# Kernel optimization log

Measured on AMD Instinct MI355X. Metric: run time of the kernel, lower is better.

## Reference

```python
import jax, jax.numpy as jnp
import numpy as np


def setup_inputs() -> dict:
    key = jax.random.key(0)
    k1, k2, k3, k4 = jax.random.split(key, 4)
    B, T, E, H, D = 4, 2048, 1024, 16, 64
    x = jax.random.normal(k1, (B, T, E), dtype=jnp.float32)
    # wv stored as [E, H*D] so y = x @ wv (math-equivalent to nn.Linear weight.T)
    wv = jax.random.normal(k2, (E, H * D), dtype=jnp.float32) * (1.0 / E) ** 0.5
    wr = jax.random.normal(k3, (H, E, T), dtype=jnp.float32) * (2.0 / E) ** 0.5
    wo = jax.random.normal(k4, (H * D, E), dtype=jnp.float32) * (1.0 / (H * D)) ** 0.5
    return {"x": x, "wv": wv, "wr": wr, "wo": wo}


def reference(x, wv, wr, wo):
    B, T, E = x.shape
    H = wr.shape[0]
    HD = wv.shape[1]
    D = HD // H
    # values: [B, H, T, D]
    v = (x @ wv).reshape(B, T, H, D).transpose(0, 2, 1, 3)
    # per-key scores, identical for every query row: s[b,h,k]
    s = jnp.einsum('bte,het->bht', x, wr[:, :, :T]) / jnp.sqrt(jnp.asarray(D, x.dtype))
    # causal softmax over keys k<=q with scores shared across queries reduces to
    # a prefix-softmax-weighted cumulative sum over V (exact same math, O(T)):
    # out[q] = sum_{k<=q} exp(s_k - m) v_k / sum_{k<=q} exp(s_k - m)
    m = jnp.max(s, axis=-1, keepdims=True)          # global max is a valid stable shift
    e = jnp.exp(s - m)                              # [B,H,T]
    num = jnp.cumsum(e[..., None] * v, axis=2)      # [B,H,T,D]
    den = jnp.cumsum(e, axis=2)[..., None]          # [B,H,T,1]
    out = num / den                                 # [B,H,T,D]
    out = out.transpose(0, 2, 1, 3).reshape(B, T, HD)
    return out @ wo
```

## Files before the change

### kernel.cpp

```cpp
#include <hip/hip_runtime.h>
#include <stdint.h>

typedef unsigned short u16;
typedef __attribute__((ext_vector_type(8))) short short8;
typedef __attribute__((ext_vector_type(8))) unsigned short ushort8v;
typedef __attribute__((ext_vector_type(4))) float f32x4;

#define B_  4
#define T_  2048
#define E_  1024
#define H_  16
#define D_  64
#define HD_ 1024
#define BT_ (B_*T_)
#define TC_ 64
#define NC_ (T_/TC_)
#define SG_ 32
#define SEB_ (E_/SG_)
#define SHB_ 2

__device__ __forceinline__ u16 f2b(float f) {
  uint32_t u = __float_as_uint(f);
  uint32_t r = (u + 0x7FFFu + ((u >> 16) & 1u)) >> 16;
  return (u16)r;
}
__device__ __forceinline__ float b2f(u16 u) {
  return __uint_as_float(((uint32_t)u) << 16);
}

__global__ __launch_bounds__(256) void prep_all(const float* __restrict__ x,
                                                const float* __restrict__ wv,
                                                const float* __restrict__ wo,
                                                u16* __restrict__ xb,
                                                u16* __restrict__ xTb8,
                                                u16* __restrict__ wvT,
                                                u16* __restrict__ woT) {
  __shared__ float tile[64][65];
  const int bid = blockIdx.x;
  if (bid < 2048) {
    const int b = bid >> 9, rest = bid & 511;
    const int t0 = (rest >> 4) * 64, e0 = (rest & 15) * 64;
    const int c4 = (threadIdx.x & 15) * 4;
    const int rw = threadIdx.x >> 4;
#pragma unroll
    for (int r = 0; r < 4; ++r) {
      const int row = r * 16 + rw;
      const float4 v4 = *reinterpret_cast<const float4*>(
          &x[((size_t)b * T_ + t0 + row) * E_ + e0 + c4]);
      tile[row][c4 + 0] = v4.x; tile[row][c4 + 1] = v4.y;
      tile[row][c4 + 2] = v4.z; tile[row][c4 + 3] = v4.w;
      ushort4 o;
      o.x = f2b(v4.x); o.y = f2b(v4.y); o.z = f2b(v4.z); o.w = f2b(v4.w);
      *reinterpret_cast<ushort4*>(&xb[((size_t)(b * T_ + t0 + row)) * E_ + e0 + c4]) = o;
    }
    __syncthreads();
    const int tl = threadIdx.x & 63;
    const int eg = threadIdx.x >> 6;
#pragma unroll
    for (int p = 0; p < 2; ++p) {
      const int egg = eg + p * 4;
      ushort8v o;
#pragma unroll
      for (int j = 0; j < 8; ++j) o[j] = f2b(tile[tl][egg * 8 + j]);
      *reinterpret_cast<ushort8v*>(
          &xTb8[((size_t)(b * (E_ / 8) + (e0 >> 3) + egg) * T_ + t0 + tl) * 8]) = o;
    }
  } else {
    const int k = bid - 2048;
    const float* in = (k >> 8) ? wo : wv;
    u16* out = (k >> 8) ? woT : wvT;
    const int r0 = ((k >> 4) & 15) * 64, c0 = (k & 15) * 64;
    const int tx = threadIdx.x & 63, ty = threadIdx.x >> 6;
#pragma unroll
    for (int r = 0; r < 16; ++r) {
      int row = r * 4 + ty;
      tile[row][tx] = in[(size_t)(r0 + row) * 1024 + c0 + tx];
    }
    __syncthreads();
#pragma unroll
    for (int r = 0; r < 16; ++r) {
      int row = r * 4 + ty;
      out[(size_t)(c0 + row) * 1024 + r0 + tx] = f2b(tile[tx][row]);
    }
  }
}

template <int OUT_BF16>
__global__ __launch_bounds__(256) void gemm_bt(const u16* __restrict__ A,
                                               const u16* __restrict__ Bt,
                                               float* __restrict__ Cf,
                                               u16* __restrict__ Cb,
                                               int M, int N, int K) {
  __shared__ __align__(16) u16 As[2][128 * 64];
  __shared__ __align__(16) u16 Bs[2][128 * 64];
  const int tid  = threadIdx.x;
  const int lane = tid & 63;
  const int wave = tid >> 6;
  const int wr_  = wave >> 1, wc_ = wave & 1;

  const int nwg = gridDim.x * gridDim.y;
  const int bid = blockIdx.y * gridDim.x + blockIdx.x;
  const int cpx = nwg >> 3;
  const int swz = (bid & 7) * cpx + (bid >> 3);
  const int bx = swz % gridDim.x, by = swz / gridDim.x;
  const int brow = by * 128;
  const int bcol = bx * 128;
  const int l15 = lane & 15, l4 = lane >> 4;

  f32x4 acc[4][4];
  const f32x4 zero = {0.f, 0.f, 0.f, 0.f};
#pragma unroll
  for (int i = 0; i < 4; ++i)
#pragma unroll
    for (int j = 0; j < 4; ++j) acc[i][j] = zero;

  auto stage = [&](int kt, int buf) {
    const int k0 = kt * 64;
#pragma unroll
    for (int s2 = 0; s2 < 4; ++s2) {
      const int c = s2 * 256 + tid;
      const int row = c >> 3, g = c & 7;
      const int gs = g ^ (row & 7);
      const u16* ga = A  + (size_t)(brow + row) * K + k0 + gs * 8;
      const u16* gb = Bt + (size_t)(bcol + row) * K + k0 + gs * 8;
      u16* la = &As[buf][(size_t)(s2 * 256 + wave * 64) * 8];
      u16* lb = &Bs[buf][(size_t)(s2 * 256 + wave * 64) * 8];
      __builtin_amdgcn_global_load_lds((const __attribute__((address_space(1))) void*)ga,
                                       (__attribute__((address_space(3))) void*)la,
                                       16, 0, 0);
      __builtin_amdgcn_global_load_lds((const __attribute__((address_space(1))) void*)gb,
                                       (__attribute__((address_space(3))) void*)lb,
                                       16, 0, 0);
    }
  };

  const int NK = K / 64;
  stage(0, 0);
  __syncthreads();

  int cur = 0;
  for (int kt = 0; kt < NK; ++kt) {
    if (kt + 1 < NK) stage(kt + 1, cur ^ 1);

    short8 af[2][4], bfr[2][4];
#pragma unroll
    for (int kk = 0; kk < 2; ++kk) {
      const int sg = (kk * 4 + l4) ^ (l15 & 7);
#pragma unroll
      for (int mi = 0; mi < 4; ++mi)
        af[kk][mi] = *reinterpret_cast<const short8*>(
            &As[cur][(wr_ * 64 + mi * 16 + l15) * 64 + sg * 8]);
#pragma unroll
      for (int ni = 0; ni < 4; ++ni)
        bfr[kk][ni] = *reinterpret_cast<const short8*>(
            &Bs[cur][(wc_ * 64 + ni * 16 + l15) * 64 + sg * 8]);
    }
    __builtin_amdgcn_s_setprio(1);
#pragma unroll
    for (int kk = 0; kk < 2; ++kk)
#pragma unroll
      for (int mi = 0; mi < 4; ++mi)
#pragma unroll
        for (int ni = 0; ni < 4; ++ni)
          acc[mi][ni] = __builtin_amdgcn_mfma_f32_16x16x32_bf16(af[kk][mi], bfr[kk][ni],
                                                                acc[mi][ni], 0, 0, 0);
    __builtin_amdgcn_s_setprio(0);
    __syncthreads();
    cur ^= 1;
  }

#pragma unroll
  for (int mi = 0; mi < 4; ++mi) {
#pragma unroll
    for (int ni = 0; ni < 4; ++ni) {
      const int col = bcol + wc_ * 64 + ni * 16 + l15;
#pragma unroll
      for (int j = 0; j < 4; ++j) {
        const int row = brow + wr_ * 64 + mi * 16 + l4 * 4 + j;
        if (OUT_BF16) Cb[(size_t)row * N + col] = f2b(acc[mi][ni][j]);
        else          Cf[(size_t)row * N + col] = acc[mi][ni][j];
      }
    }
  }
}

__global__ __launch_bounds__(256) void score_partial(const u16* __restrict__ xTb8,
                                                     const float* __restrict__ wr,
                                                     u16* __restrict__ partial) {
  const int t  = blockIdx.x * 256 + threadIdx.x;
  const int g  = blockIdx.y;
  const int h0 = blockIdx.z * SHB_;
  float acc[4][SHB_];
#pragma unroll
  for (int b = 0; b < 4; ++b)
#pragma unroll
    for (int hh = 0; hh < SHB_; ++hh) acc[b][hh] = 0.f;

#pragma unroll
  for (int e8 = 0; e8 < SEB_ / 8; ++e8) {
    const int eb = g * (SEB_ / 8) + e8;
    ushort8v xv[4];
#pragma unroll
    for (int b = 0; b < 4; ++b)
      xv[b] = *reinterpret_cast<const ushort8v*>(
          &xTb8[((size_t)(b * (E_ / 8) + eb) * T_ + t) * 8]);
#pragma unroll
    for (int j = 0; j < 8; ++j) {
      const int e = eb * 8 + j;
      float xf[4];
#pragma unroll
      for (int b = 0; b < 4; ++b) xf[b] = b2f(xv[b][j]);
#pragma unroll
      for (int hh = 0; hh < SHB_; ++hh) {
        const float w = wr[((size_t)(h0 + hh) * E_ + e) * T_ + t];
#pragma unroll
        for (int b = 0; b < 4; ++b) acc[b][hh] = fmaf(xf[b], w, acc[b][hh]);
      }
    }
  }
  u16* pp = partial + (size_t)g * (B_ * H_ * T_);
#pragma unroll
  for (int b = 0; b < 4; ++b)
#pragma unroll
    for (int hh = 0; hh < SHB_; ++hh)
      pp[((size_t)b * H_ + h0 + hh) * T_ + t] = f2b(acc[b][hh] * 0.125f);
}

__global__ __launch_bounds__(256) void chunk_sums(const u16* __restrict__ partial,
                                                  const u16* __restrict__ v,
                                                  float* __restrict__ s,
                                                  float* __restrict__ sev,
                                                  float* __restrict__ se,
                                                  float* __restrict__ mc) {
  const int bh = blockIdx.y;
  const int b = bh >> 4, h = bh & 15;
  const int w = threadIdx.x >> 6, d = threadIdx.x & 63;
  const int c = blockIdx.x * 4 + w;
  const int t = blockIdx.x * 256 + threadIdx.x;

  float sv = 0.f;
#pragma unroll
  for (int g = 0; g < SG_; ++g)
    sv += b2f(partial[(size_t)g * (B_ * H_ * T_) + (size_t)bh * T_ + t]);
  s[(size_t)bh * T_ + t] = sv;

  __shared__ float es[4][64];
  es[w][d] = sv;

  float lm = sv;
#pragma unroll
  for (int off = 1; off < 64; off <<= 1) lm = fmaxf(lm, __shfl_xor(lm, off, 64));

  const u16* vp = v + ((size_t)(b * T_ + c * TC_)) * HD_ + h * D_ + d;
  float acc = 0.f, ae = 0.f;
#pragma unroll 8
  for (int tt = 0; tt < TC_; ++tt) {
    float e = __expf(es[w][tt] - lm);
    acc = fmaf(e, b2f(vp[(size_t)tt * HD_]), acc);
    ae += e;
  }
  sev[((size_t)bh * NC_ + c) * D_ + d] = acc;
  if (d == 0) { se[bh * NC_ + c] = ae; mc[bh * NC_ + c] = lm; }
}

__global__ __launch_bounds__(256) void chunk_scan(const float* __restrict__ s,
                                                  const u16* __restrict__ v,
                                                  const float* __restrict__ sev,
                                                  const float* __restrict__ se,
                                                  const float* __restrict__ mc,
                                                  u16* __restrict__ attn) {
  const int bh = blockIdx.y;
  const int b = bh >> 4, h = bh & 15;
  const int w = threadIdx.x >> 6, d = threadIdx.x & 63;
  const int c = blockIdx.x * 4 + w;
  const float* mcp = mc + bh * NC_;

  float gm = (d < NC_) ? mcp[d] : -1e30f;
#pragma unroll
  for (int off = 1; off < 64; off <<= 1) gm = fmaxf(gm, __shfl_xor(gm, off, 64));

  const float* sevp = sev + (size_t)bh * NC_ * D_;
  const float* sep  = se + bh * NC_;
  float pn = 0.f, pd = 0.f;
  for (int c2 = 0; c2 < c; ++c2) {
    float f = __expf(mcp[c2] - gm);
    pn = fmaf(sevp[(size_t)c2 * D_ + d], f, pn);
    pd = fmaf(sep[c2], f, pd);
  }

  const float* sp = s + (size_t)bh * T_ + c * TC_;
  const u16* vp = v + ((size_t)(b * T_ + c * TC_)) * HD_ + h * D_ + d;
  u16* ap = attn + ((size_t)(b * T_ + c * TC_)) * HD_ + h * D_ + d;
#pragma unroll 8
  for (int tt = 0; tt < TC_; ++tt) {
    float e = __expf(sp[tt] - gm);
    pn = fmaf(e, b2f(vp[(size_t)tt * HD_]), pn);
    pd += e;
    ap[(size_t)tt * HD_] = f2b(__fdividef(pn, pd));
  }
}

extern "C" void kernel_launch(void* const* d_in, const int* in_sizes, int n_in,
                              void* d_out, int out_size, void* d_ws, size_t ws_size,
                              hipStream_t stream) {
  const float* x  = (const float*)d_in[0];
  const float* wv = (const float*)d_in[1];
  const float* wr = (const float*)d_in[2];
  const float* wo = (const float*)d_in[3];
  float* out = (float*)d_out;

  char* ws = (char*)d_ws;
  size_t off = 0;
  auto alloc = [&](size_t bytes) {
    void* p = ws + off;
    off += (bytes + 255) & ~(size_t)255;
    return p;
  };
  u16*   xb   = (u16*)  alloc((size_t)BT_ * E_ * 2);
  u16*   xTb8 = (u16*)  alloc((size_t)B_ * E_ * T_ * 2);
  u16*   wvT  = (u16*)  alloc((size_t)HD_ * E_ * 2);
  u16*   woT  = (u16*)  alloc((size_t)E_ * HD_ * 2);
  u16*   vv   = (u16*)  alloc((size_t)BT_ * HD_ * 2);
  u16*   attn = (u16*)  alloc((size_t)BT_ * HD_ * 2);
  float* s    = (float*)alloc((size_t)B_ * H_ * T_ * 4);
  float* sev  = (float*)alloc((size_t)B_ * H_ * NC_ * D_ * 4);
  float* se   = (float*)alloc((size_t)B_ * H_ * NC_ * 4);
  float* mc   = (float*)alloc((size_t)B_ * H_ * NC_ * 4);
  u16*   part = (u16*)  alloc((size_t)SG_ * B_ * H_ * T_ * 2);

  prep_all<<<2560, 256, 0, stream>>>(x, wv, wo, xb, xTb8, wvT, woT);

  gemm_bt<1><<<dim3(HD_ / 128, BT_ / 128), 256, 0, stream>>>(xb, wvT, nullptr, vv, BT_, HD_, E_);

  score_partial<<<dim3(T_ / 256, SG_, H_ / SHB_), 256, 0, stream>>>(xTb8, wr, part);

  chunk_sums<<<dim3(NC_ / 4, B_ * H_), 256, 0, stream>>>(part, vv, s, sev, se, mc);
  chunk_scan<<<dim3(NC_ / 4, B_ * H_), 256, 0, stream>>>(s, vv, sev, se, mc, attn);

  gemm_bt<0><<<dim3(E_ / 128, BT_ / 128), 256, 0, stream>>>(attn, woT, out, nullptr, BT_, E_, HD_);
}
```

Before: 119.2 us.

## Fuse value GEMM and score partial kernel into warp-specialized single launch

Merges the x@wv GEMM and the memory-bound score_partial kernel into one 512-thread kernel. Waves 0-3 run the MFMA GEMM tile and waves 4-7 compute score partial sums from wr, so compute-bound and bandwidth-bound work can share each CU concurrently. The score waves join each of the GEMM's __syncthreads barriers, 16 times plus one initial barrier, to keep barrier counts matched. This couples the two workloads' progress and raises register and LDS pressure per block.

```diff
diff --git a/kernel.cpp b/kernel.cpp
--- a/kernel.cpp
+++ b/kernel.cpp
@@ -85,14 +85,162 @@
   }
 }
 
-template <int OUT_BF16>
-__global__ __launch_bounds__(256) void gemm_bt(const u16* __restrict__ A,
-                                               const u16* __restrict__ Bt,
-                                               float* __restrict__ Cf,
-                                               u16* __restrict__ Cb,
-                                               int M, int N, int K) {
+__global__ __launch_bounds__(512, 4) void gemm1_score(
+    const u16* __restrict__ A,
+    const u16* __restrict__ Bt,
+    u16* __restrict__ Cb,
+    const u16* __restrict__ xTb8,
+    const float* __restrict__ wr,
+    u16* __restrict__ partial) {
   __shared__ __align__(16) u16 As[2][128 * 64];
   __shared__ __align__(16) u16 Bs[2][128 * 64];
+  const int tid  = threadIdx.x;
+  const int K = 1024, N = 1024;
+
+  if (tid < 256) {
+    const int lane = tid & 63;
+    const int wave = tid >> 6;
+    const int wr_  = wave >> 1, wc_ = wave & 1;
+
+    const int nwg = gridDim.x;
+    const int bid = blockIdx.x;
+    const int cpx = nwg >> 3;
+    const int swz = (bid & 7) * cpx + (bid >> 3);
+    const int bx = swz & 7, by = swz >> 3;
+    const int brow = by * 128;
+    const int bcol = bx * 128;
+    const int l15 = lane & 15, l4 = lane >> 4;
+
+    f32x4 acc[4][4];
+    const f32x4 zero = {0.f, 0.f, 0.f, 0.f};
+#pragma unroll
+    for (int i = 0; i < 4; ++i)
+#pragma unroll
+      for (int j = 0; j < 4; ++j) acc[i][j] = zero;
+
+    auto stage = [&](int kt, int buf) {
+      const int k0 = kt * 64;
+#pragma unroll
+      for (int s2 = 0; s2 < 4; ++s2) {
+        const int c = s2 * 256 + tid;
+        const int row = c >> 3, g = c & 7;
+        const int gs = g ^ (row & 7);
+        const u16* ga = A  + (size_t)(brow + row) * K + k0 + gs * 8;
+        const u16* gb = Bt + (size_t)(bcol + row) * K + k0 + gs * 8;
+        u16* la = &As[buf][(size_t)(s2 * 256 + wave * 64) * 8];
+        u16* lb = &Bs[buf][(size_t)(s2 * 256 + wave * 64) * 8];
+        __builtin_amdgcn_global_load_lds((const __attribute__((address_space(1))) void*)ga,
+                                         (__attribute__((address_space(3))) void*)la,
+                                         16, 0, 0);
+        __builtin_amdgcn_global_load_lds((const __attribute__((address_space(1))) void*)gb,
+                                         (__attribute__((address_space(3))) void*)lb,
+                                         16, 0, 0);
+      }
+    };
+
+    stage(0, 0);
+    __syncthreads();
+    int cur = 0;
+    for (int kt = 0; kt < 16; ++kt) {
+      if (kt + 1 < 16) stage(kt + 1, cur ^ 1);
+
+      short8 af[2][4], bfr[2][4];
+#pragma unroll
+      for (int kk = 0; kk < 2; ++kk) {
+        const int sg = (kk * 4 + l4) ^ (l15 & 7);
+#pragma unroll
+        for (int mi = 0; mi < 4; ++mi)
+          af[kk][mi] = *reinterpret_cast<const short8*>(
+              &As[cur][(wr_ * 64 + mi * 16 + l15) * 64 + sg * 8]);
+#pragma unroll
+        for (int ni = 0; ni < 4; ++ni)
+          bfr[kk][ni] = *reinterpret_cast<const short8*>(
+              &Bs[cur][(wc_ * 64 + ni * 16 + l15) * 64 + sg * 8]);
+      }
+      __builtin_amdgcn_s_setprio(1);
+#pragma unroll
+      for (int kk = 0; kk < 2; ++kk)
+#pragma unroll
+        for (int mi = 0; mi < 4; ++mi)
+#pragma unroll
+          for (int ni = 0; ni < 4; ++ni)
+            acc[mi][ni] = __builtin_amdgcn_mfma_f32_16x16x32_bf16(af[kk][mi], bfr[kk][ni],
+                                                                  acc[mi][ni], 0, 0, 0);
+      __builtin_amdgcn_s_setprio(0);
+      __syncthreads();
+      cur ^= 1;
+    }
+
+#pragma unroll
+    for (int mi = 0; mi < 4; ++mi) {
+#pragma unroll
+      for (int ni = 0; ni < 4; ++ni) {
+        const int col = bcol + wc_ * 64 + ni * 16 + l15;
+#pragma unroll
+        for (int j = 0; j < 4; ++j) {
+          const int row = brow + wr_ * 64 + mi * 16 + l4 * 4 + j;
+          Cb[(size_t)row * N + col] = f2b(acc[mi][ni][j]);
+        }
+      }
+    }
+  } else {
+    const int lane = tid & 63;
+    const int unit = blockIdx.x * 4 + ((tid >> 6) - 4);
+    const int hz  = unit >> 8;
+    const int g   = (unit >> 3) & 31;
+    const int tb  = (unit & 7) * 256;
+    const int h0  = hz * SHB_;
+
+    __syncthreads();
+
+    float acc[4][SHB_];
+    for (int seg = 0; seg < 16; ++seg) {
+      const int tc = seg >> 2, e8 = seg & 3;
+      const int t = tb + tc * 64 + lane;
+      if (e8 == 0) {
+#pragma unroll
+        for (int b = 0; b < 4; ++b)
+#pragma unroll
+          for (int hh = 0; hh < SHB_; ++hh) acc[b][hh] = 0.f;
+      }
+      const int eb = g * 4 + e8;
+      ushort8v xv[4];
+#pragma unroll
+      for (int b = 0; b < 4; ++b)
+        xv[b] = *reinterpret_cast<const ushort8v*>(
+            &xTb8[((size_t)(b * (E_ / 8) + eb) * T_ + t) * 8]);
+#pragma unroll
+      for (int j = 0; j < 8; ++j) {
+        const int e = eb * 8 + j;
+        float xf[4];
+#pragma unroll
+        for (int b = 0; b < 4; ++b) xf[b] = b2f(xv[b][j]);
+#pragma unroll
+        for (int hh = 0; hh < SHB_; ++hh) {
+          const float w = wr[((size_t)(h0 + hh) * E_ + e) * T_ + t];
+#pragma unroll
+          for (int b = 0; b < 4; ++b) acc[b][hh] = fmaf(xf[b], w, acc[b][hh]);
+        }
+      }
+      if (e8 == 3) {
+        u16* pp = partial + (size_t)g * (B_ * H_ * T_);
+#pragma unroll
+        for (int b = 0; b < 4; ++b)
+#pragma unroll
+          for (int hh = 0; hh < SHB_; ++hh)
+            pp[((size_t)b * H_ + h0 + hh) * T_ + t] = f2b(acc[b][hh] * 0.125f);
+      }
+      __syncthreads();
+    }
+  }
+}
+
+__global__ __launch_bounds__(256) void gemm_out(const u16* __restrict__ A,
+                                                const u16* __restrict__ Bt,
+                                                float* __restrict__ Cf) {
+  __shared__ __align__(16) u16 As[2][128 * 64];
+  __shared__ __align__(16) u16 Bs[2][128 * 64];
+  const int K = 1024, N = 1024;
   const int tid  = threadIdx.x;
   const int lane = tid & 63;
   const int wave = tid >> 6;
@@ -134,13 +282,11 @@
     }
   };
 
-  const int NK = K / 64;
   stage(0, 0);
   __syncthreads();
-
   int cur = 0;
-  for (int kt = 0; kt < NK; ++kt) {
-    if (kt + 1 < NK) stage(kt + 1, cur ^ 1);
+  for (int kt = 0; kt < 16; ++kt) {
+    if (kt + 1 < 16) stage(kt + 1, cur ^ 1);
 
     short8 af[2][4], bfr[2][4];
 #pragma unroll
@@ -177,53 +323,10 @@
 #pragma unroll
       for (int j = 0; j < 4; ++j) {
         const int row = brow + wr_ * 64 + mi * 16 + l4 * 4 + j;
-        if (OUT_BF16) Cb[(size_t)row * N + col] = f2b(acc[mi][ni][j]);
-        else          Cf[(size_t)row * N + col] = acc[mi][ni][j];
-      }
-    }
-  }
-}
-
-__global__ __launch_bounds__(256) void score_partial(const u16* __restrict__ xTb8,
-                                                     const float* __restrict__ wr,
-                                                     u16* __restrict__ partial) {
-  const int t  = blockIdx.x * 256 + threadIdx.x;
-  const int g  = blockIdx.y;
-  const int h0 = blockIdx.z * SHB_;
-  float acc[4][SHB_];
-#pragma unroll
-  for (int b = 0; b < 4; ++b)
-#pragma unroll
-    for (int hh = 0; hh < SHB_; ++hh) acc[b][hh] = 0.f;
-
-#pragma unroll
-  for (int e8 = 0; e8 < SEB_ / 8; ++e8) {
-    const int eb = g * (SEB_ / 8) + e8;
-    ushort8v xv[4];
-#pragma unroll
-    for (int b = 0; b < 4; ++b)
-      xv[b] = *reinterpret_cast<const ushort8v*>(
-          &xTb8[((size_t)(b * (E_ / 8) + eb) * T_ + t) * 8]);
-#pragma unroll
-    for (int j = 0; j < 8; ++j) {
-      const int e = eb * 8 + j;
-      float xf[4];
-#pragma unroll
-      for (int b = 0; b < 4; ++b) xf[b] = b2f(xv[b][j]);
-#pragma unroll
-      for (int hh = 0; hh < SHB_; ++hh) {
-        const float w = wr[((size_t)(h0 + hh) * E_ + e) * T_ + t];
-#pragma unroll
-        for (int b = 0; b < 4; ++b) acc[b][hh] = fmaf(xf[b], w, acc[b][hh]);
-      }
-    }
-  }
-  u16* pp = partial + (size_t)g * (B_ * H_ * T_);
-#pragma unroll
-  for (int b = 0; b < 4; ++b)
-#pragma unroll
-    for (int hh = 0; hh < SHB_; ++hh)
-      pp[((size_t)b * H_ + h0 + hh) * T_ + t] = f2b(acc[b][hh] * 0.125f);
+        Cf[(size_t)row * N + col] = acc[mi][ni][j];
+      }
+    }
+  }
 }
 
 __global__ __launch_bounds__(256) void chunk_sums(const u16* __restrict__ partial,
@@ -330,12 +433,10 @@
 
   prep_all<<<2560, 256, 0, stream>>>(x, wv, wo, xb, xTb8, wvT, woT);
 
-  gemm_bt<1><<<dim3(HD_ / 128, BT_ / 128), 256, 0, stream>>>(xb, wvT, nullptr, vv, BT_, HD_, E_);
-
-  score_partial<<<dim3(T_ / 256, SG_, H_ / SHB_), 256, 0, stream>>>(xTb8, wr, part);
+  gemm1_score<<<512, 512, 0, stream>>>(xb, wvT, vv, xTb8, wr, part);
 
   chunk_sums<<<dim3(NC_ / 4, B_ * H_), 256, 0, stream>>>(part, vv, s, sev, se, mc);
   chunk_scan<<<dim3(NC_ / 4, B_ * H_), 256, 0, stream>>>(s, vv, sev, se, mc, attn);
 
-  gemm_bt<0><<<dim3(E_ / 128, BT_ / 128), 256, 0, stream>>>(attn, woT, out, nullptr, BT_, E_, HD_);
-}
+  gemm_out<<<dim3(HD_ / 128, BT_ / 128), 256, 0, stream>>>(attn, woT, out);
+}
```

Result: slower. 160.1 us (+34.4%).
